# Performance work log

Hardware: AMD Instinct MI355X
Metric: run time of the kernel (lower is better)

The kernel has to match this reference:

```python
import jax, jax.numpy as jnp
import numpy as np

HID = 128

def _sage(h, src, dst, Wl, bl, Wr, n):
    # PyG SAGEConv (mean aggr): out = lin_l(mean_{j in N(i)} h_j) + lin_r(h_i)
    msg = h[src]                                   # [E, H] gather
    s = jax.ops.segment_sum(msg, dst, num_segments=n)
    cnt = jax.ops.segment_sum(jnp.ones_like(dst, dtype=h.dtype), dst, num_segments=n)
    m = s / jnp.maximum(cnt, 1.0)[:, None]
    return m @ Wl + bl + h @ Wr

def setup_inputs() -> dict:
    key = jax.random.key(0)
    ks = jax.random.split(key, 20)
    NP, NC, E = 20000, 80000, 1600000
    N = NP + NC
    inp = {
        'x_pol_dyn': jax.random.normal(ks[0], (NP, 64), jnp.float32),
        'pol_state_idx': jax.random.randint(ks[1], (NP,), 0, 50),
        'x_comp_dyn': jax.random.normal(ks[2], (NC, 96), jnp.float32),
        'comp_sector_idx': jax.random.randint(ks[3], (NC,), 0, 12),
        'comp_ind_idx': jax.random.randint(ks[4], (NC,), 0, 150),
        'edge_index': jax.random.randint(ks[5], (2, E), 0, N),
        'state_emb': jax.random.normal(ks[6], (50, 8), jnp.float32) * 0.1,
        'sector_emb': jax.random.normal(ks[7], (12, 8), jnp.float32) * 0.1,
        'ind_emb': jax.random.normal(ks[8], (150, 8), jnp.float32) * 0.1,
        'W_pol': jax.random.normal(ks[9], (64 + 8, HID), jnp.float32) * 0.05,
        'b_pol': jnp.zeros((HID,), jnp.float32),
        'W_comp': jax.random.normal(ks[10], (96 + 16, HID), jnp.float32) * 0.05,
        'b_comp': jnp.zeros((HID,), jnp.float32),
        'Wl1': jax.random.normal(ks[11], (HID, HID), jnp.float32) * 0.05,
        'bl1': jnp.zeros((HID,), jnp.float32),
        'Wr1': jax.random.normal(ks[12], (HID, HID), jnp.float32) * 0.05,
        'Wl2': jax.random.normal(ks[13], (HID, HID), jnp.float32) * 0.05,
        'bl2': jnp.zeros((HID,), jnp.float32),
        'Wr2': jax.random.normal(ks[14], (HID, HID), jnp.float32) * 0.05,
    }
    return inp

def reference(x_pol_dyn, pol_state_idx, x_comp_dyn, comp_sector_idx, comp_ind_idx,
              edge_index, state_emb, sector_emb, ind_emb,
              W_pol, b_pol, W_comp, b_comp, Wl1, bl1, Wr1, Wl2, bl2, Wr2):
    pol_feat = jnp.concatenate([x_pol_dyn, state_emb[pol_state_idx]], axis=-1)
    comp_feat = jnp.concatenate([x_comp_dyn, sector_emb[comp_sector_idx], ind_emb[comp_ind_idx]], axis=-1)
    h_pol = jax.nn.relu(pol_feat @ W_pol + b_pol)
    h_comp = jax.nn.relu(comp_feat @ W_comp + b_comp)
    # dropout is identity in eval mode
    h = jnp.concatenate([h_pol, h_comp], axis=0)
    n = h.shape[0]
    src, dst = edge_index[0], edge_index[1]
    h = jax.nn.relu(_sage(h, src, dst, Wl1, bl1, Wr1, n))
    h = _sage(h, src, dst, Wl2, bl2, Wr2, n)
    np_ = h_pol.shape[0]
    return h[:np_], h[np_:]
```

## Files before the change

### kernel.cpp

```cpp
#include <hip/hip_runtime.h>

#define NP 20000
#define NC 80000
#define NN 100000
#define NE 1600000
#define HD 128
#define MAXDEG 64
#define BKT 391
#define BINB 391

typedef unsigned short ushort_t;
typedef unsigned int uint_t;

typedef __attribute__((ext_vector_type(8))) short bf16x8;
typedef __attribute__((ext_vector_type(4))) float f32x4;

__device__ __forceinline__ ushort_t f2bf(float f) {
  uint_t u = __builtin_bit_cast(uint_t, f);
  u = (u + 0x7FFF + ((u >> 16) & 1)) >> 16;
  return (ushort_t)u;
}
__device__ __forceinline__ float bf_lo(uint_t p) {
  return __builtin_bit_cast(float, p << 16);
}
__device__ __forceinline__ float bf_hi(uint_t p) {
  return __builtin_bit_cast(float, p & 0xFFFF0000u);
}
__device__ __forceinline__ uint4 pack8(float4 lo, float4 hi) {
  ushort_t t[8];
  t[0] = f2bf(lo.x); t[1] = f2bf(lo.y); t[2] = f2bf(lo.z); t[3] = f2bf(lo.w);
  t[4] = f2bf(hi.x); t[5] = f2bf(hi.y); t[6] = f2bf(hi.z); t[7] = f2bf(hi.w);
  return *(uint4*)t;
}

__device__ __forceinline__ void pack_tile(const float* __restrict__ W,
                                          ushort_t* __restrict__ P, int KF,
                                          int KB, int task) {
  int t = task / (KB * 64);
  int rem = task - t * KB * 64;
  int kb = rem >> 6;
  int lane = rem & 63;
  int k0 = kb * 32 + ((lane >> 4) << 3);
  int c = t * 16 + (lane & 15);
  ushort_t tmp[8];
#pragma unroll
  for (int j = 0; j < 8; ++j) {
    int k = k0 + j;
    tmp[j] = (k < KF) ? f2bf(W[(size_t)k * HD + c]) : (ushort_t)0;
  }
  *(uint4*)(P + (size_t)task * 8) = *(uint4*)tmp;
}

#define PACKB 46
__global__ __launch_bounds__(256) void prep_k(
    const int* __restrict__ dst, int* __restrict__ bcnt,
    const float* __restrict__ Wl1, const float* __restrict__ Wr1,
    const float* __restrict__ Wl2, const float* __restrict__ Wr2,
    const float* __restrict__ W_comp, const float* __restrict__ W_pol,
    ushort_t* __restrict__ wl1p, ushort_t* __restrict__ wr1p,
    ushort_t* __restrict__ wl2p, ushort_t* __restrict__ wr2p,
    ushort_t* __restrict__ wcompp, ushort_t* __restrict__ wpolp) {
  __shared__ int hist[BKT];
  int blk = blockIdx.x;
  int tid = threadIdx.x;
  if (blk < BINB) {
    for (int t = tid; t < BKT; t += 256) hist[t] = 0;
    __syncthreads();
    int base = blk * 4096;
#pragma unroll
    for (int q = 0; q < 16; ++q) {
      int e = base + q * 256 + tid;
      if (e < NE) atomicAdd(&hist[dst[e] >> 8], 1);
    }
    __syncthreads();
    for (int t = tid; t < BKT; t += 256)
      if (hist[t] > 0) atomicAdd(&bcnt[t], hist[t]);
    return;
  }
  int pb = blk - BINB;
  if (pb < 8) pack_tile(Wl1, wl1p, 128, 4, pb * 256 + tid);
  else if (pb < 16) pack_tile(Wr1, wr1p, 128, 4, (pb - 8) * 256 + tid);
  else if (pb < 24) pack_tile(Wl2, wl2p, 128, 4, (pb - 16) * 256 + tid);
  else if (pb < 32) pack_tile(Wr2, wr2p, 128, 4, (pb - 24) * 256 + tid);
  else if (pb < 40) pack_tile(W_comp, wcompp, 112, 4, (pb - 32) * 256 + tid);
  else pack_tile(W_pol, wpolp, 72, 3, (pb - 40) * 256 + tid);
}

__global__ __launch_bounds__(512) void scan_k(const int* __restrict__ bcnt,
                                              int* __restrict__ bstart,
                                              int* __restrict__ bfill) {
  __shared__ int s[512];
  int t = threadIdx.x;
  int v = (t < BKT) ? bcnt[t] : 0;
  s[t] = v;
  __syncthreads();
  for (int off = 1; off < 512; off <<= 1) {
    int x = (t >= off) ? s[t - off] : 0;
    __syncthreads();
    s[t] += x;
    __syncthreads();
  }
  if (t < BKT) {
    int st = s[t] - v;
    bstart[t] = st;
    bfill[t] = st;
  }
}

#define COMP_E (NC / 128)
#define POL_E ((NP + 127) / 128)
__global__ __launch_bounds__(512) void bin_enc_k(
    const int* __restrict__ src, const int* __restrict__ dst,
    int* __restrict__ bfill, uint_t* __restrict__ ebuf,
    const float* __restrict__ x_comp, const int* __restrict__ sec,
    const int* __restrict__ ind, const float* __restrict__ semb,
    const float* __restrict__ iemb, const ushort_t* __restrict__ wcompp,
    const float* __restrict__ b_comp,
    const float* __restrict__ x_pol, const int* __restrict__ sidx,
    const float* __restrict__ stemb, const ushort_t* __restrict__ wpolp,
    const float* __restrict__ b_pol,
    ushort_t* __restrict__ h0) {
  __shared__ int hist[BKT];
  __shared__ int lscan[BKT];
  __shared__ int gbase[BKT];
  __shared__ int sv[512];
  __shared__ uint2 stage[4096];
  int blk = blockIdx.x;
  int tid = threadIdx.x;

  if (blk < BINB) {
    for (int t = tid; t < BKT; t += 512) hist[t] = 0;
    __syncthreads();
    int base = blk * 4096;
    int cntE = min(4096, NE - base);
    int ss[8], dd[8], rr[8];
#pragma unroll
    for (int q = 0; q < 8; ++q) {
      int e = base + q * 512 + tid;
      if (e < NE) {
        dd[q] = dst[e];
        ss[q] = src[e];
        rr[q] = atomicAdd(&hist[dd[q] >> 8], 1);
      } else {
        dd[q] = -1;
      }
    }
    __syncthreads();
    int hv = (tid < BKT) ? hist[tid] : 0;
    sv[tid] = hv;
    __syncthreads();
    for (int off = 1; off < 512; off <<= 1) {
      int x = (tid >= off) ? sv[tid - off] : 0;
      __syncthreads();
      sv[tid] += x;
      __syncthreads();
    }
    if (tid < BKT) {
      lscan[tid] = sv[tid] - hv;
      if (hv > 0) gbase[tid] = atomicAdd(&bfill[tid], hv);
    }
    __syncthreads();
#pragma unroll
    for (int q = 0; q < 8; ++q) {
      if (dd[q] >= 0) {
        int bb = dd[q] >> 8;
        stage[lscan[bb] + rr[q]] = make_uint2((uint_t)ss[q], (uint_t)dd[q]);
      }
    }
    __syncthreads();
    for (int j = tid; j < cntE; j += 512) {
      uint2 v = stage[j];
      int bb = v.y >> 8;
      ebuf[gbase[bb] + (j - lscan[bb])] = (v.x << 8) | (v.y & 255u);
    }
    return;
  }
  int lane = tid & 63;
  int wv = tid >> 6;
  int n16 = lane & 15, quad = lane >> 4;
  if (blk < BINB + COMP_E) {
    int rowbase = (blk - BINB) * 128 + wv * 16;
    int node = rowbase + n16;
    const float4* xr = (const float4*)(x_comp + (size_t)node * 96);
    uint4 a[4];
#pragma unroll
    for (int kb = 0; kb < 3; ++kb)
      a[kb] = pack8(xr[kb * 8 + quad * 2], xr[kb * 8 + quad * 2 + 1]);
    if (quad == 0) {
      const float4* er = (const float4*)(semb + (size_t)sec[node] * 8);
      a[3] = pack8(er[0], er[1]);
    } else if (quad == 1) {
      const float4* er = (const float4*)(iemb + (size_t)ind[node] * 8);
      a[3] = pack8(er[0], er[1]);
    } else {
      a[3] = make_uint4(0, 0, 0, 0);
    }
    const bf16x8* W = (const bf16x8*)wcompp;
    ushort_t* hb = h0 + (size_t)NP * HD;
#pragma unroll
    for (int t = 0; t < 8; ++t) {
      float bias = b_comp[t * 16 + n16];
      f32x4 acc = {bias, bias, bias, bias};
#pragma unroll
      for (int kb = 0; kb < 4; ++kb)
        acc = __builtin_amdgcn_mfma_f32_16x16x32_bf16(
            __builtin_bit_cast(bf16x8, a[kb]), W[(t * 4 + kb) * 64 + lane],
            acc, 0, 0, 0);
      int r0 = rowbase + quad * 4;
      int c = t * 16 + n16;
#pragma unroll
      for (int r = 0; r < 4; ++r)
        hb[(size_t)(r0 + r) * HD + c] = f2bf(fmaxf(acc[r], 0.f));
    }
    return;
  }
  {
    int rowbase = (blk - BINB - COMP_E) * 128 + wv * 16;
    if (rowbase >= NP) return;
    int node = rowbase + n16;
    const float4* xr = (const float4*)(x_pol + (size_t)node * 64);
    uint4 a[3];
#pragma unroll
    for (int kb = 0; kb < 2; ++kb)
      a[kb] = pack8(xr[kb * 8 + quad * 2], xr[kb * 8 + quad * 2 + 1]);
    if (quad == 0) {
      const float4* er = (const float4*)(stemb + (size_t)sidx[node] * 8);
      a[2] = pack8(er[0], er[1]);
    } else {
      a[2] = make_uint4(0, 0, 0, 0);
    }
    const bf16x8* W = (const bf16x8*)wpolp;
#pragma unroll
    for (int t = 0; t < 8; ++t) {
      float bias = b_pol[t * 16 + n16];
      f32x4 acc = {bias, bias, bias, bias};
#pragma unroll
      for (int kb = 0; kb < 3; ++kb)
        acc = __builtin_amdgcn_mfma_f32_16x16x32_bf16(
            __builtin_bit_cast(bf16x8, a[kb]), W[(t * 3 + kb) * 64 + lane],
            acc, 0, 0, 0);
      int r0 = rowbase + quad * 4;
      int c = t * 16 + n16;
#pragma unroll
      for (int r = 0; r < 4; ++r)
        h0[(size_t)(r0 + r) * HD + c] = f2bf(fmaxf(acc[r], 0.f));
    }
  }
}

__global__ __launch_bounds__(512) void build_k(const uint_t* __restrict__ ebuf,
                                               const int* __restrict__ bstart,
                                               const int* __restrict__ bcnt,
                                               int* __restrict__ col,
                                               int* __restrict__ cnt) {
  __shared__ int lcnt[256];
  int tid = threadIdx.x;
  int b = blockIdx.x;
  if (tid < 256) lcnt[tid] = 0;
  __syncthreads();
  int st = bstart[b];
  int cb = bcnt[b];
  for (int off = tid; off < cb; off += 512) {
    uint_t v = ebuf[st + off];
    int nl = v & 255u;
    int p = atomicAdd(&lcnt[nl], 1);
    if (p < MAXDEG) col[(size_t)((b << 8) | nl) * MAXDEG + p] = (int)(v >> 8);
  }
  __syncthreads();
  if (tid < 256) {
    int node = (b << 8) + tid;
    if (node < NN) cnt[node] = lcnt[tid];
  }
}

__global__ __launch_bounds__(256) void aggregate_k(
    const ushort_t* __restrict__ hbf, const int* __restrict__ cnt,
    const int* __restrict__ col, ushort_t* __restrict__ mbf) {
  const uint4* hrow = (const uint4*)hbf;
  int lane = threadIdx.x & 63;
  int iA = (blockIdx.x * 4 + (threadIdx.x >> 6)) * 2;
  int iB = iA + 1;
  int dA = min(cnt[iA], MAXDEG);
  int dB = min(cnt[iB], MAXDEG);
  int grp = lane >> 4;
  int l16 = lane & 15;
  float accA[8] = {0.f, 0.f, 0.f, 0.f, 0.f, 0.f, 0.f, 0.f};
  float accB[8] = {0.f, 0.f, 0.f, 0.f, 0.f, 0.f, 0.f, 0.f};
  int mycA = (lane < dA) ? col[(size_t)iA * MAXDEG + lane] : 0;
  int mycB = (lane < dB) ? col[(size_t)iB * MAXDEG + lane] : 0;
  int nch = (max(dA, dB) + 15) >> 4;
  for (int ch = 0; ch < nch; ++ch) {
    int j0 = ch * 16;
    uint4 pA[4], pB[4];
    bool vA[4], vB[4];
#pragma unroll
    for (int q = 0; q < 4; ++q) {
      int e = j0 + q * 4 + grp;
      vA[q] = e < dA;
      int s = __shfl(mycA, vA[q] ? e : 0);
      pA[q] = hrow[(size_t)s * 16 + l16];
    }
#pragma unroll
    for (int q = 0; q < 4; ++q) {
      int e = j0 + q * 4 + grp;
      vB[q] = e < dB;
      int s = __shfl(mycB, vB[q] ? e : 0);
      pB[q] = hrow[(size_t)s * 16 + l16];
    }
#pragma unroll
    for (int q = 0; q < 4; ++q) {
      if (vA[q]) {
        accA[0] += bf_lo(pA[q].x); accA[1] += bf_hi(pA[q].x);
        accA[2] += bf_lo(pA[q].y); accA[3] += bf_hi(pA[q].y);
        accA[4] += bf_lo(pA[q].z); accA[5] += bf_hi(pA[q].z);
        accA[6] += bf_lo(pA[q].w); accA[7] += bf_hi(pA[q].w);
      }
      if (vB[q]) {
        accB[0] += bf_lo(pB[q].x); accB[1] += bf_hi(pB[q].x);
        accB[2] += bf_lo(pB[q].y); accB[3] += bf_hi(pB[q].y);
        accB[4] += bf_lo(pB[q].z); accB[5] += bf_hi(pB[q].z);
        accB[6] += bf_lo(pB[q].w); accB[7] += bf_hi(pB[q].w);
      }
    }
  }
#pragma unroll
  for (int k = 0; k < 8; ++k) {
    accA[k] += __shfl_xor(accA[k], 16);
    accA[k] += __shfl_xor(accA[k], 32);
    accB[k] += __shfl_xor(accB[k], 16);
    accB[k] += __shfl_xor(accB[k], 32);
  }
  if (grp == 0) {
    float inv = 1.f / (float)max(dA, 1);
    ushort_t t[8];
#pragma unroll
    for (int k = 0; k < 8; ++k) t[k] = f2bf(accA[k] * inv);
    *(uint4*)(mbf + (size_t)iA * HD + l16 * 8) = *(uint4*)t;
  } else if (grp == 1) {
    float inv = 1.f / (float)max(dB, 1);
    ushort_t t[8];
#pragma unroll
    for (int k = 0; k < 8; ++k) t[k] = f2bf(accB[k] * inv);
    *(uint4*)(mbf + (size_t)iB * HD + l16 * 8) = *(uint4*)t;
  }
}

__global__ __launch_bounds__(256) void sage_mfma_k(
    const ushort_t* __restrict__ mb, const ushort_t* __restrict__ hb,
    const ushort_t* __restrict__ Wlp, const float* __restrict__ bl,
    const ushort_t* __restrict__ Wrp, float* __restrict__ outf,
    ushort_t* __restrict__ outb, int relu) {
  int lane = threadIdx.x & 63;
  int rowbase = blockIdx.x * 64 + (threadIdx.x >> 6) * 16;
  if (rowbase >= NN) return;
  int n16 = lane & 15, quad = lane >> 4;
  const uint4* mrow = (const uint4*)(mb + (size_t)(rowbase + n16) * HD);
  const uint4* hrow = (const uint4*)(hb + (size_t)(rowbase + n16) * HD);
  uint4 am[4], ah[4];
#pragma unroll
  for (int kb = 0; kb < 4; ++kb) {
    am[kb] = mrow[kb * 4 + quad];
    ah[kb] = hrow[kb * 4 + quad];
  }
  const bf16x8* WL = (const bf16x8*)Wlp;
  const bf16x8* WR = (const bf16x8*)Wrp;
#pragma unroll
  for (int t = 0; t < 8; ++t) {
    float bias = bl[t * 16 + n16];
    f32x4 acc = {bias, bias, bias, bias};
#pragma unroll
    for (int kb = 0; kb < 4; ++kb)
      acc = __builtin_amdgcn_mfma_f32_16x16x32_bf16(
          __builtin_bit_cast(bf16x8, am[kb]), WL[(t * 4 + kb) * 64 + lane],
          acc, 0, 0, 0);
#pragma unroll
    for (int kb = 0; kb < 4; ++kb)
      acc = __builtin_amdgcn_mfma_f32_16x16x32_bf16(
          __builtin_bit_cast(bf16x8, ah[kb]), WR[(t * 4 + kb) * 64 + lane],
          acc, 0, 0, 0);
    int r0 = rowbase + quad * 4;
    int c = t * 16 + n16;
#pragma unroll
    for (int r = 0; r < 4; ++r) {
      float v = acc[r];
      if (relu) v = fmaxf(v, 0.f);
      if (outb)
        outb[(size_t)(r0 + r) * HD + c] = f2bf(v);
      else
        outf[(size_t)(r0 + r) * HD + c] = v;
    }
  }
}

extern "C" void kernel_launch(void* const* d_in, const int* in_sizes, int n_in,
                              void* d_out, int out_size, void* d_ws,
                              size_t ws_size, hipStream_t stream) {
  const float* x_pol = (const float*)d_in[0];
  const int* pol_state_idx = (const int*)d_in[1];
  const float* x_comp = (const float*)d_in[2];
  const int* comp_sector = (const int*)d_in[3];
  const int* comp_ind = (const int*)d_in[4];
  const int* edge = (const int*)d_in[5];
  const float* state_emb = (const float*)d_in[6];
  const float* sector_emb = (const float*)d_in[7];
  const float* ind_emb = (const float*)d_in[8];
  const float* W_pol = (const float*)d_in[9];
  const float* b_pol = (const float*)d_in[10];
  const float* W_comp = (const float*)d_in[11];
  const float* b_comp = (const float*)d_in[12];
  const float* Wl1 = (const float*)d_in[13];
  const float* bl1 = (const float*)d_in[14];
  const float* Wr1 = (const float*)d_in[15];
  const float* Wl2 = (const float*)d_in[16];
  const float* bl2 = (const float*)d_in[17];
  const float* Wr2 = (const float*)d_in[18];

  const int* src = edge;
  const int* dst = edge + NE;

  const size_t HBYTES = (size_t)NN * HD * sizeof(ushort_t);
  char* ws = (char*)d_ws;
  ushort_t* m_bf = (ushort_t*)ws;
  ushort_t* h0_bf = (ushort_t*)(ws + HBYTES);
  ushort_t* h1_bf = (ushort_t*)(ws + 2 * HBYTES);
  int* col = (int*)(ws + 3 * HBYTES);
  uint_t* ebuf = (uint_t*)(col + (size_t)NN * MAXDEG);
  int* cnt = (int*)(ebuf + NE);
  ushort_t* wl1p = (ushort_t*)(cnt + NN);
  ushort_t* wr1p = wl1p + 16384;
  ushort_t* wl2p = wr1p + 16384;
  ushort_t* wr2p = wl2p + 16384;
  ushort_t* wcompp = wr2p + 16384;
  ushort_t* wpolp = wcompp + 16384;
  int* bcnt = (int*)(wpolp + 12288);
  int* bstart = bcnt + BKT;
  int* bfill = bstart + BKT;

  float* out_f = (float*)d_out;

  hipMemsetAsync(bcnt, 0, BKT * sizeof(int), stream);

  prep_k<<<BINB + PACKB, 256, 0, stream>>>(dst, bcnt, Wl1, Wr1, Wl2, Wr2,
                                           W_comp, W_pol, wl1p, wr1p, wl2p,
                                           wr2p, wcompp, wpolp);
  scan_k<<<1, 512, 0, stream>>>(bcnt, bstart, bfill);
  bin_enc_k<<<BINB + COMP_E + POL_E, 512, 0, stream>>>(
      src, dst, bfill, ebuf, x_comp, comp_sector, comp_ind, sector_emb,
      ind_emb, wcompp, b_comp, x_pol, pol_state_idx, state_emb, wpolp, b_pol,
      h0_bf);
  build_k<<<BKT, 512, 0, stream>>>(ebuf, bstart, bcnt, col, cnt);

  const int GB = (NN + 63) / 64;
  aggregate_k<<<NN / 8, 256, 0, stream>>>(h0_bf, cnt, col, m_bf);
  sage_mfma_k<<<GB, 256, 0, stream>>>(m_bf, h0_bf, wl1p, bl1, wr1p, nullptr,
                                      h1_bf, 1);

  aggregate_k<<<NN / 8, 256, 0, stream>>>(h1_bf, cnt, col, m_bf);
  sage_mfma_k<<<GB, 256, 0, stream>>>(m_bf, h1_bf, wl2p, bl2, wr2p, out_f,
                                      nullptr, 0);
}
```

Measured before the change: 343.8 us.

## Replace atomic bucket fill with per-block histogram prefix scan

Each binning block now writes its per-bucket histogram to a transposed global table instead of atomically adding into global bucket counts. A new per-bucket scan kernel turns the table into per-block exclusive offsets and bucket totals. The scatter pass then takes deterministic write bases from those offsets rather than from atomicAdd on a fill counter. This drops a memset and the global atomics and makes edge order stable, at the cost of an extra small kernel launch and a 391x391 table.

```diff
diff --git a/kernel.cpp b/kernel.cpp
--- a/kernel.cpp
+++ b/kernel.cpp
@@ -53,7 +53,7 @@
 
 #define PACKB 46
 __global__ __launch_bounds__(256) void prep_k(
-    const int* __restrict__ dst, int* __restrict__ bcnt,
+    const int* __restrict__ dst, int* __restrict__ hist2t,
     const float* __restrict__ Wl1, const float* __restrict__ Wr1,
     const float* __restrict__ Wl2, const float* __restrict__ Wr2,
     const float* __restrict__ W_comp, const float* __restrict__ W_pol,
@@ -74,7 +74,7 @@
     }
     __syncthreads();
     for (int t = tid; t < BKT; t += 256)
-      if (hist[t] > 0) atomicAdd(&bcnt[t], hist[t]);
+      hist2t[(size_t)t * BINB + blk] = hist[t];
     return;
   }
   int pb = blk - BINB;
@@ -86,9 +86,29 @@
   else pack_tile(W_pol, wpolp, 72, 3, (pb - 40) * 256 + tid);
 }
 
+__global__ __launch_bounds__(64) void scanA_k(int* __restrict__ hist2t,
+                                              int* __restrict__ bcnt) {
+  int t = blockIdx.x;
+  int lane = threadIdx.x;
+  int* base = hist2t + (size_t)t * BINB;
+  int carry = 0;
+  for (int c = 0; c < 7; ++c) {
+    int i = c * 64 + lane;
+    int orig = (i < BINB) ? base[i] : 0;
+    int v = orig;
+#pragma unroll
+    for (int off = 1; off < 64; off <<= 1) {
+      int u = __shfl_up(v, off);
+      if (lane >= off) v += u;
+    }
+    if (i < BINB) base[i] = v - orig + carry;
+    carry += __shfl(v, 63);
+  }
+  if (lane == 0) bcnt[t] = carry;
+}
+
 __global__ __launch_bounds__(512) void scan_k(const int* __restrict__ bcnt,
-                                              int* __restrict__ bstart,
-                                              int* __restrict__ bfill) {
+                                              int* __restrict__ bstart) {
   __shared__ int s[512];
   int t = threadIdx.x;
   int v = (t < BKT) ? bcnt[t] : 0;
@@ -100,18 +120,15 @@
     s[t] += x;
     __syncthreads();
   }
-  if (t < BKT) {
-    int st = s[t] - v;
-    bstart[t] = st;
-    bfill[t] = st;
-  }
+  if (t < BKT) bstart[t] = s[t] - v;
 }
 
 #define COMP_E (NC / 128)
 #define POL_E ((NP + 127) / 128)
 __global__ __launch_bounds__(512) void bin_enc_k(
     const int* __restrict__ src, const int* __restrict__ dst,
-    int* __restrict__ bfill, uint_t* __restrict__ ebuf,
+    const int* __restrict__ bstart, const int* __restrict__ hist2t,
+    uint_t* __restrict__ ebuf,
     const float* __restrict__ x_comp, const int* __restrict__ sec,
     const int* __restrict__ ind, const float* __restrict__ semb,
     const float* __restrict__ iemb, const ushort_t* __restrict__ wcompp,
@@ -157,7 +174,7 @@
     }
     if (tid < BKT) {
       lscan[tid] = sv[tid] - hv;
-      if (hv > 0) gbase[tid] = atomicAdd(&bfill[tid], hv);
+      gbase[tid] = bstart[tid] + hist2t[(size_t)tid * BINB + blk];
     }
     __syncthreads();
 #pragma unroll
@@ -434,20 +451,19 @@
   ushort_t* wpolp = wcompp + 16384;
   int* bcnt = (int*)(wpolp + 12288);
   int* bstart = bcnt + BKT;
-  int* bfill = bstart + BKT;
+  int* hist2t = bstart + BKT;
 
   float* out_f = (float*)d_out;
 
-  hipMemsetAsync(bcnt, 0, BKT * sizeof(int), stream);
-
-  prep_k<<<BINB + PACKB, 256, 0, stream>>>(dst, bcnt, Wl1, Wr1, Wl2, Wr2,
+  prep_k<<<BINB + PACKB, 256, 0, stream>>>(dst, hist2t, Wl1, Wr1, Wl2, Wr2,
                                            W_comp, W_pol, wl1p, wr1p, wl2p,
                                            wr2p, wcompp, wpolp);
-  scan_k<<<1, 512, 0, stream>>>(bcnt, bstart, bfill);
+  scanA_k<<<BKT, 64, 0, stream>>>(hist2t, bcnt);
+  scan_k<<<1, 512, 0, stream>>>(bcnt, bstart);
   bin_enc_k<<<BINB + COMP_E + POL_E, 512, 0, stream>>>(
-      src, dst, bfill, ebuf, x_comp, comp_sector, comp_ind, sector_emb,
-      ind_emb, wcompp, b_comp, x_pol, pol_state_idx, state_emb, wpolp, b_pol,
-      h0_bf);
+      src, dst, bstart, hist2t, ebuf, x_comp, comp_sector, comp_ind,
+      sector_emb, ind_emb, wcompp, b_comp, x_pol, pol_state_idx, state_emb,
+      wpolp, b_pol, h0_bf);
   build_k<<<BKT, 512, 0, stream>>>(ebuf, bstart, bcnt, col, cnt);
 
   const int GB = (NN + 63) / 64;
```

New measurement: 333.8 us. 2.9% less time.

## Replace bucketed counting-sort CSR build with direct global atomic slot insertion

Applied to the files above, without the earlier changes.

Removes the three-pass bucket histogram, scan and build pipeline and instead has each edge atomically claim a slot in its destination's fixed-width column list in global memory, fused into the encoder kernel. This cuts several kernel launches, the intermediate edge buffer and its extra reads and writes. In exchange it issues 1.6M scattered global atomics and scattered column writes, and neighbor order within each node is now nondeterministic. Weight packing is split into its own small kernel.

```diff
diff --git a/kernel.cpp b/kernel.cpp
--- a/kernel.cpp
+++ b/kernel.cpp
@@ -6,8 +6,6 @@
 #define NE 1600000
 #define HD 128
 #define MAXDEG 64
-#define BKT 391
-#define BINB 391
 
 typedef unsigned short ushort_t;
 typedef unsigned int uint_t;
@@ -51,67 +49,29 @@
   *(uint4*)(P + (size_t)task * 8) = *(uint4*)tmp;
 }
 
-#define PACKB 46
-__global__ __launch_bounds__(256) void prep_k(
-    const int* __restrict__ dst, int* __restrict__ bcnt,
+__global__ __launch_bounds__(512) void wpack_k(
     const float* __restrict__ Wl1, const float* __restrict__ Wr1,
     const float* __restrict__ Wl2, const float* __restrict__ Wr2,
     const float* __restrict__ W_comp, const float* __restrict__ W_pol,
     ushort_t* __restrict__ wl1p, ushort_t* __restrict__ wr1p,
     ushort_t* __restrict__ wl2p, ushort_t* __restrict__ wr2p,
     ushort_t* __restrict__ wcompp, ushort_t* __restrict__ wpolp) {
-  __shared__ int hist[BKT];
-  int blk = blockIdx.x;
+  int pb = blockIdx.x;
   int tid = threadIdx.x;
-  if (blk < BINB) {
-    for (int t = tid; t < BKT; t += 256) hist[t] = 0;
-    __syncthreads();
-    int base = blk * 4096;
-#pragma unroll
-    for (int q = 0; q < 16; ++q) {
-      int e = base + q * 256 + tid;
-      if (e < NE) atomicAdd(&hist[dst[e] >> 8], 1);
-    }
-    __syncthreads();
-    for (int t = tid; t < BKT; t += 256)
-      if (hist[t] > 0) atomicAdd(&bcnt[t], hist[t]);
-    return;
-  }
-  int pb = blk - BINB;
-  if (pb < 8) pack_tile(Wl1, wl1p, 128, 4, pb * 256 + tid);
-  else if (pb < 16) pack_tile(Wr1, wr1p, 128, 4, (pb - 8) * 256 + tid);
-  else if (pb < 24) pack_tile(Wl2, wl2p, 128, 4, (pb - 16) * 256 + tid);
-  else if (pb < 32) pack_tile(Wr2, wr2p, 128, 4, (pb - 24) * 256 + tid);
-  else if (pb < 40) pack_tile(W_comp, wcompp, 112, 4, (pb - 32) * 256 + tid);
-  else pack_tile(W_pol, wpolp, 72, 3, (pb - 40) * 256 + tid);
-}
-
-__global__ __launch_bounds__(512) void scan_k(const int* __restrict__ bcnt,
-                                              int* __restrict__ bstart,
-                                              int* __restrict__ bfill) {
-  __shared__ int s[512];
-  int t = threadIdx.x;
-  int v = (t < BKT) ? bcnt[t] : 0;
-  s[t] = v;
-  __syncthreads();
-  for (int off = 1; off < 512; off <<= 1) {
-    int x = (t >= off) ? s[t - off] : 0;
-    __syncthreads();
-    s[t] += x;
-    __syncthreads();
-  }
-  if (t < BKT) {
-    int st = s[t] - v;
-    bstart[t] = st;
-    bfill[t] = st;
-  }
-}
-
+  if (pb < 4) pack_tile(Wl1, wl1p, 128, 4, pb * 512 + tid);
+  else if (pb < 8) pack_tile(Wr1, wr1p, 128, 4, (pb - 4) * 512 + tid);
+  else if (pb < 12) pack_tile(Wl2, wl2p, 128, 4, (pb - 8) * 512 + tid);
+  else if (pb < 16) pack_tile(Wr2, wr2p, 128, 4, (pb - 12) * 512 + tid);
+  else if (pb < 20) pack_tile(W_comp, wcompp, 112, 4, (pb - 16) * 512 + tid);
+  else pack_tile(W_pol, wpolp, 72, 3, (pb - 20) * 512 + tid);
+}
+
+#define EDGEB 782
 #define COMP_E (NC / 128)
 #define POL_E ((NP + 127) / 128)
-__global__ __launch_bounds__(512) void bin_enc_k(
+__global__ __launch_bounds__(512) void mega_k(
     const int* __restrict__ src, const int* __restrict__ dst,
-    int* __restrict__ bfill, uint_t* __restrict__ ebuf,
+    int* __restrict__ cnt, int* __restrict__ col,
     const float* __restrict__ x_comp, const int* __restrict__ sec,
     const int* __restrict__ ind, const float* __restrict__ semb,
     const float* __restrict__ iemb, const ushort_t* __restrict__ wcompp,
@@ -120,66 +80,27 @@
     const float* __restrict__ stemb, const ushort_t* __restrict__ wpolp,
     const float* __restrict__ b_pol,
     ushort_t* __restrict__ h0) {
-  __shared__ int hist[BKT];
-  __shared__ int lscan[BKT];
-  __shared__ int gbase[BKT];
-  __shared__ int sv[512];
-  __shared__ uint2 stage[4096];
   int blk = blockIdx.x;
   int tid = threadIdx.x;
-
-  if (blk < BINB) {
-    for (int t = tid; t < BKT; t += 512) hist[t] = 0;
-    __syncthreads();
-    int base = blk * 4096;
-    int cntE = min(4096, NE - base);
-    int ss[8], dd[8], rr[8];
-#pragma unroll
-    for (int q = 0; q < 8; ++q) {
-      int e = base + q * 512 + tid;
+  if (blk < EDGEB) {
+    int base = blk * 2048 + tid;
+#pragma unroll
+    for (int q = 0; q < 4; ++q) {
+      int e = base + q * 512;
       if (e < NE) {
-        dd[q] = dst[e];
-        ss[q] = src[e];
-        rr[q] = atomicAdd(&hist[dd[q] >> 8], 1);
-      } else {
-        dd[q] = -1;
+        int d = dst[e];
+        int s = src[e];
+        int p = atomicAdd(&cnt[d], 1);
+        if (p < MAXDEG) col[(size_t)d * MAXDEG + p] = s;
       }
-    }
-    __syncthreads();
-    int hv = (tid < BKT) ? hist[tid] : 0;
-    sv[tid] = hv;
-    __syncthreads();
-    for (int off = 1; off < 512; off <<= 1) {
-      int x = (tid >= off) ? sv[tid - off] : 0;
-      __syncthreads();
-      sv[tid] += x;
-      __syncthreads();
-    }
-    if (tid < BKT) {
-      lscan[tid] = sv[tid] - hv;
-      if (hv > 0) gbase[tid] = atomicAdd(&bfill[tid], hv);
-    }
-    __syncthreads();
-#pragma unroll
-    for (int q = 0; q < 8; ++q) {
-      if (dd[q] >= 0) {
-        int bb = dd[q] >> 8;
-        stage[lscan[bb] + rr[q]] = make_uint2((uint_t)ss[q], (uint_t)dd[q]);
-      }
-    }
-    __syncthreads();
-    for (int j = tid; j < cntE; j += 512) {
-      uint2 v = stage[j];
-      int bb = v.y >> 8;
-      ebuf[gbase[bb] + (j - lscan[bb])] = (v.x << 8) | (v.y & 255u);
     }
     return;
   }
   int lane = tid & 63;
   int wv = tid >> 6;
   int n16 = lane & 15, quad = lane >> 4;
-  if (blk < BINB + COMP_E) {
-    int rowbase = (blk - BINB) * 128 + wv * 16;
+  if (blk < EDGEB + COMP_E) {
+    int rowbase = (blk - EDGEB) * 128 + wv * 16;
     int node = rowbase + n16;
     const float4* xr = (const float4*)(x_comp + (size_t)node * 96);
     uint4 a[4];
@@ -215,7 +136,7 @@
     return;
   }
   {
-    int rowbase = (blk - BINB - COMP_E) * 128 + wv * 16;
+    int rowbase = (blk - EDGEB - COMP_E) * 128 + wv * 16;
     if (rowbase >= NP) return;
     int node = rowbase + n16;
     const float4* xr = (const float4*)(x_pol + (size_t)node * 64);
@@ -245,31 +166,6 @@
       for (int r = 0; r < 4; ++r)
         h0[(size_t)(r0 + r) * HD + c] = f2bf(fmaxf(acc[r], 0.f));
     }
-  }
-}
-
-__global__ __launch_bounds__(512) void build_k(const uint_t* __restrict__ ebuf,
-                                               const int* __restrict__ bstart,
-                                               const int* __restrict__ bcnt,
-                                               int* __restrict__ col,
-                                               int* __restrict__ cnt) {
-  __shared__ int lcnt[256];
-  int tid = threadIdx.x;
-  int b = blockIdx.x;
-  if (tid < 256) lcnt[tid] = 0;
-  __syncthreads();
-  int st = bstart[b];
-  int cb = bcnt[b];
-  for (int off = tid; off < cb; off += 512) {
-    uint_t v = ebuf[st + off];
-    int nl = v & 255u;
-    int p = atomicAdd(&lcnt[nl], 1);
-    if (p < MAXDEG) col[(size_t)((b << 8) | nl) * MAXDEG + p] = (int)(v >> 8);
-  }
-  __syncthreads();
-  if (tid < 256) {
-    int node = (b << 8) + tid;
-    if (node < NN) cnt[node] = lcnt[tid];
   }
 }
 
@@ -400,7 +296,6 @@
   const float* x_comp = (const float*)d_in[2];
   const int* comp_sector = (const int*)d_in[3];
   const int* comp_ind = (const int*)d_in[4];
-  const int* edge = (const int*)d_in[5];
   const float* state_emb = (const float*)d_in[6];
   const float* sector_emb = (const float*)d_in[7];
   const float* ind_emb = (const float*)d_in[8];
@@ -415,8 +310,8 @@
   const float* bl2 = (const float*)d_in[17];
   const float* Wr2 = (const float*)d_in[18];
 
-  const int* src = edge;
-  const int* dst = edge + NE;
+  const int* src = (const int*)d_in[5];
+  const int* dst = ((const int*)d_in[5]) + NE;
 
   const size_t HBYTES = (size_t)NN * HD * sizeof(ushort_t);
   char* ws = (char*)d_ws;
@@ -424,31 +319,24 @@
   ushort_t* h0_bf = (ushort_t*)(ws + HBYTES);
   ushort_t* h1_bf = (ushort_t*)(ws + 2 * HBYTES);
   int* col = (int*)(ws + 3 * HBYTES);
-  uint_t* ebuf = (uint_t*)(col + (size_t)NN * MAXDEG);
-  int* cnt = (int*)(ebuf + NE);
+  int* cnt = col + (size_t)NN * MAXDEG;
   ushort_t* wl1p = (ushort_t*)(cnt + NN);
   ushort_t* wr1p = wl1p + 16384;
   ushort_t* wl2p = wr1p + 16384;
   ushort_t* wr2p = wl2p + 16384;
   ushort_t* wcompp = wr2p + 16384;
   ushort_t* wpolp = wcompp + 16384;
-  int* bcnt = (int*)(wpolp + 12288);
-  int* bstart = bcnt + BKT;
-  int* bfill = bstart + BKT;
 
   float* out_f = (float*)d_out;
 
-  hipMemsetAsync(bcnt, 0, BKT * sizeof(int), stream);
-
-  prep_k<<<BINB + PACKB, 256, 0, stream>>>(dst, bcnt, Wl1, Wr1, Wl2, Wr2,
-                                           W_comp, W_pol, wl1p, wr1p, wl2p,
-                                           wr2p, wcompp, wpolp);
-  scan_k<<<1, 512, 0, stream>>>(bcnt, bstart, bfill);
-  bin_enc_k<<<BINB + COMP_E + POL_E, 512, 0, stream>>>(
-      src, dst, bfill, ebuf, x_comp, comp_sector, comp_ind, sector_emb,
-      ind_emb, wcompp, b_comp, x_pol, pol_state_idx, state_emb, wpolp, b_pol,
-      h0_bf);
-  build_k<<<BKT, 512, 0, stream>>>(ebuf, bstart, bcnt, col, cnt);
+  hipMemsetAsync(cnt, 0, NN * sizeof(int), stream);
+
+  wpack_k<<<23, 512, 0, stream>>>(Wl1, Wr1, Wl2, Wr2, W_comp, W_pol, wl1p,
+                                  wr1p, wl2p, wr2p, wcompp, wpolp);
+
+  mega_k<<<EDGEB + COMP_E + POL_E, 512, 0, stream>>>(
+      src, dst, cnt, col, x_comp, comp_sector, comp_ind, sector_emb, ind_emb,
+      wcompp, b_comp, x_pol, pol_state_idx, state_emb, wpolp, b_pol, h0_bf);
 
   const int GB = (NN + 63) / 64;
   aggregate_k<<<NN / 8, 256, 0, stream>>>(h0_bf, cnt, col, m_bf);
```

After: 447.6 us. 1.3x slower.
